# Optimization experiments

Measured on AMD Instinct MI355X. Metric: run time of the kernel, lower is better.

Reference implementation:

```python
import jax, jax.numpy as jnp
import numpy as np

D_MODEL = 2048
NUM_HEADS = 32
D_HEAD = D_MODEL // NUM_HEADS
L = 2048


def setup_inputs() -> dict:
    key = jax.random.key(0)
    ks = jax.random.split(key, 9)
    s = 0.02  # init scale
    return {
        "X": jax.random.normal(ks[0], (L, D_MODEL), dtype=jnp.float32),
        "Wq_w": jax.random.normal(ks[1], (D_MODEL, D_MODEL), jnp.float32) * s,
        "Wq_b": jax.random.normal(ks[2], (D_MODEL,), jnp.float32) * s,
        "Wk_w": jax.random.normal(ks[3], (D_MODEL, D_MODEL), jnp.float32) * s,
        "Wk_b": jax.random.normal(ks[4], (D_MODEL,), jnp.float32) * s,
        "Wv_w": jax.random.normal(ks[5], (D_MODEL, D_MODEL), jnp.float32) * s,
        "Wv_b": jax.random.normal(ks[6], (D_MODEL,), jnp.float32) * s,
        "Wo_w": jax.random.normal(ks[7], (D_MODEL, D_MODEL), jnp.float32) * s,
        "Wo_b": jax.random.normal(ks[8], (D_MODEL,), jnp.float32) * s,
    }


def reference(X, Wq_w, Wq_b, Wk_w, Wk_b, Wv_w, Wv_b, Wo_w, Wo_b):
    # torch.nn.Linear: y = x @ W.T + b
    seq = X.shape[0]
    Q = (X @ Wq_w.T + Wq_b).reshape(seq, D_HEAD, NUM_HEADS)  # (L, d, h)
    K = (X @ Wk_w.T + Wk_b).reshape(seq, D_HEAD, NUM_HEADS)
    V = (X @ Wv_w.T + Wv_b).reshape(seq, D_HEAD, NUM_HEADS)
    # scores[l, m, h] = sum_d Q[l,d,h] * K[m,d,h]; note scale is sqrt(d_model),
    # faithful to the source (not sqrt(d_head)).
    scores = jnp.einsum('ldh,mdh->lmh', Q, K) / jnp.sqrt(jnp.float32(D_MODEL))
    attn = jax.nn.softmax(scores, axis=1)  # softmax over key axis m
    out = jnp.einsum('lmh,mdh->ldh', attn, V).reshape(seq, D_MODEL)
    return out @ Wo_w.T + Wo_b
```

## Files before the change

### kernel.cpp

```cpp
#include <hip/hip_runtime.h>
#include <hip/hip_bf16.h>
#include <stdint.h>
#include <stddef.h>

#define L_SEQ   2048
#define DM      2048
#define NH      32
#define DH      64
#define QSCALE  0.02209708691207961f
#define QS2     0.0318793579f
#define MAT_N   (L_SEQ * DM)

typedef __bf16  bf16x8 __attribute__((ext_vector_type(8)));
typedef float   f32x4  __attribute__((ext_vector_type(4)));
typedef __hip_bfloat16 bf16;

#if __has_builtin(__builtin_amdgcn_exp2f)
#define EXP2F(x) __builtin_amdgcn_exp2f(x)
#else
#define EXP2F(x) __expf((x) * 0.6931471805599453f)
#endif

__device__ __forceinline__ void gl_lds16(const bf16* g, bf16* l) {
    __builtin_amdgcn_global_load_lds(
        (const __attribute__((address_space(1))) unsigned int*)g,
        (__attribute__((address_space(3))) unsigned int*)l,
        16, 0, 0);
}

__device__ __forceinline__ void conv8s(const float* src, bf16* dst, int i, float sc) {
    float4 a = *(const float4*)(src + i);
    float4 b = *(const float4*)(src + i + 4);
    union { bf16 h[8]; uint4 u; } pk;
    pk.h[0] = __float2bfloat16(a.x * sc); pk.h[1] = __float2bfloat16(a.y * sc);
    pk.h[2] = __float2bfloat16(a.z * sc); pk.h[3] = __float2bfloat16(a.w * sc);
    pk.h[4] = __float2bfloat16(b.x * sc); pk.h[5] = __float2bfloat16(b.y * sc);
    pk.h[6] = __float2bfloat16(b.z * sc); pk.h[7] = __float2bfloat16(b.w * sc);
    *(uint4*)(dst + i) = pk.u;
}

__global__ __launch_bounds__(256)
void convert4_kernel(const float* __restrict__ s0, const float* __restrict__ s1,
                     const float* __restrict__ s2, const float* __restrict__ s3,
                     bf16* __restrict__ d0, bf16* __restrict__ d1,
                     bf16* __restrict__ d2, bf16* __restrict__ d3)
{
    const float* s; bf16* d; float sc = 1.0f;
    switch (blockIdx.y) {
        case 0:  s = s0; d = d0; break;
        case 1:  s = s1; d = d1; sc = QS2; break;
        case 2:  s = s2; d = d2; break;
        default: s = s3; d = d3; break;
    }
    const int i = (blockIdx.x * 256 + threadIdx.x) * 8;
    conv8s(s, d, i, sc);
}

__global__ __launch_bounds__(256)
void convert_wo_perm_kernel(const float* __restrict__ s, bf16* __restrict__ d)
{
    const int t   = blockIdx.x * 256 + threadIdx.x;
    const int row = t >> 8;
    const int k0  = (t & 255) * 8;
    const float* sr = s + (size_t)row * DM;
    union { bf16 h[8]; uint4 u; } pk;
#pragma unroll
    for (int j = 0; j < 8; ++j) {
        const int kp = k0 + j;
        const int k  = ((kp & 63) << 5) | (kp >> 6);
        pk.h[j] = __float2bfloat16(sr[k]);
    }
    *(uint4*)(d + (size_t)row * DM + k0) = pk.u;
}

__global__ __launch_bounds__(512)
void qkv8_gemm_kernel(const bf16* __restrict__ Xb,
                      const bf16* __restrict__ Wq, const float* __restrict__ bq,
                      const bf16* __restrict__ Wk, const float* __restrict__ bk,
                      const bf16* __restrict__ Wv, const float* __restrict__ bv,
                      bf16* __restrict__ Qws, bf16* __restrict__ Kws, bf16* __restrict__ Vws,
                      const float* __restrict__ WoSrc, bf16* __restrict__ WobDst)
{
    __shared__ bf16 lds[2 * 32768];

    const int bid = blockIdx.x;
    const int tid  = threadIdx.x;

    if (bid >= 192) {
        const int t = (bid - 192) * 512 + tid;
        const int row = t >> 4;
        const int k0base = (t & 15) * 128;
        const float* sr = WoSrc + (size_t)row * DM;
        bf16* dr = WobDst + (size_t)row * DM;
        for (int i = 0; i < 16; ++i) {
            const int k0 = k0base + i * 8;
            union { bf16 h[8]; uint4 u; } pk;
#pragma unroll
            for (int j = 0; j < 8; ++j) {
                const int kp = k0 + j;
                const int k  = ((kp & 63) << 5) | (kp >> 6);
                pk.h[j] = __float2bfloat16(sr[k]);
            }
            *(uint4*)(dr + k0) = pk.u;
        }
        return;
    }

    const int mt  = bid & 7;
    const int nt  = bid >> 3;
    const int m0  = mt << 8;
    const int ng0 = nt << 8;
    const int z   = ng0 >> 11;
    const int n0  = ng0 & 2047;
    const bf16*  W    = (z == 0) ? Wq : (z == 1) ? Wk : Wv;
    const float* bias = (z == 0) ? bq : (z == 1) ? bk : bv;

    const int lane = tid & 63;
    const int wave = tid >> 6;
    const int wm   = wave >> 2;
    const int wn   = wave & 3;
    const int grp8 = (lane >> 4) * 8;
    const int grp4 = (lane >> 4) * 4;
    const int l15  = lane & 15;
    const int axor = (l15 & 7) << 3;

    const int scol = ((tid & 7) * 8) ^ (((tid >> 3) & 7) << 3);
    const bf16* gb[8];
    int loff[8];
#pragma unroll
    for (int e = 0; e < 8; ++e) {
        const int hh  = e >> 1;
        const int row = (e & 1) * 64 + (tid >> 3);
        loff[e] = hh * 8192 + (e & 1) * 4096 + tid * 8;
        if (hh < 2) {
            gb[e] = Xb + (size_t)(m0 + hh * 128 + row) * DM + scol;
        } else {
            const int nn   = n0 + (hh - 2) * 128 + row;
            const int brow = ((nn & 63) << 5) | (nn >> 6);
            gb[e] = W + (size_t)brow * DM + scol;
        }
    }

    const bool swap  = (z == 2);
    const int  aside = swap ? 16384 : 0;
    const int  bside = swap ? 0 : 16384;
    const bf16* fa0 = lds + aside + wm * 8192 + l15 * 64;
    const bf16* fb0 = lds + bside + (wn >> 1) * 8192 + ((wn & 1) * 64 + l15) * 64;

    f32x4 acc[8][4];
    const f32x4 zero = {0.f, 0.f, 0.f, 0.f};
#pragma unroll
    for (int i = 0; i < 8; ++i)
#pragma unroll
        for (int j = 0; j < 4; ++j) acc[i][j] = zero;

#pragma unroll
    for (int e = 0; e < 8; ++e) gl_lds16(gb[e],      lds + loff[e]);
#pragma unroll
    for (int e = 0; e < 8; ++e) gl_lds16(gb[e] + 64, lds + 32768 + loff[e]);
    asm volatile("s_waitcnt vmcnt(8)" ::: "memory");
    asm volatile("s_barrier" ::: "memory");

    for (int t = 0; t < 32; ++t) {
        const int cb = (t & 1) << 15;
        const bf16* fa = fa0 + cb;
        const bf16* fb = fb0 + cb;
        const int c0 = grp8 ^ axor;
        const int c1 = (32 + grp8) ^ axor;

        bf16x8 af[8], bfr[4];
#pragma unroll
        for (int i = 0; i < 8; ++i) af[i] = *(const bf16x8*)(fa + i * 1024 + c0);
#pragma unroll
        for (int j = 0; j < 4; ++j) bfr[j] = *(const bf16x8*)(fb + j * 1024 + c0);
        asm volatile("s_barrier" ::: "memory");
        __builtin_amdgcn_s_setprio(1);
#pragma unroll
        for (int i = 0; i < 8; ++i)
#pragma unroll
            for (int j = 0; j < 4; ++j)
                acc[i][j] = __builtin_amdgcn_mfma_f32_16x16x32_bf16(af[i], bfr[j], acc[i][j], 0, 0, 0);
        __builtin_amdgcn_s_setprio(0);

#pragma unroll
        for (int i = 0; i < 8; ++i) af[i] = *(const bf16x8*)(fa + i * 1024 + c1);
#pragma unroll
        for (int j = 0; j < 4; ++j) bfr[j] = *(const bf16x8*)(fb + j * 1024 + c1);
        asm volatile("s_waitcnt lgkmcnt(0)" ::: "memory");
        asm volatile("s_barrier" ::: "memory");
        if (t + 2 < 32) {
            const int kb2 = (t + 2) << 6;
#pragma unroll
            for (int e = 0; e < 8; ++e)
                gl_lds16(gb[e] + kb2, lds + cb + loff[e]);
            asm volatile("s_waitcnt vmcnt(8)" ::: "memory");
        } else if (t == 30) {
            asm volatile("s_waitcnt vmcnt(0)" ::: "memory");
        }
        __builtin_amdgcn_s_setprio(1);
#pragma unroll
        for (int i = 0; i < 8; ++i)
#pragma unroll
            for (int j = 0; j < 4; ++j)
                acc[i][j] = __builtin_amdgcn_mfma_f32_16x16x32_bf16(af[i], bfr[j], acc[i][j], 0, 0, 0);
        __builtin_amdgcn_s_setprio(0);
        asm volatile("s_barrier" ::: "memory");
    }

    if (z == 0) {
#pragma unroll
        for (int j = 0; j < 4; ++j) {
            const int np = n0 + wn * 64 + j * 16 + l15;
            const float bb = bias[((np & 63) << 5) | (np >> 6)] * QS2;
            const size_t base = ((size_t)(np >> 6) * L_SEQ) * DH + (np & 63);
#pragma unroll
            for (int i = 0; i < 8; ++i)
#pragma unroll
                for (int r = 0; r < 4; ++r) {
                    const int m = m0 + wm * 128 + i * 16 + grp4 + r;
                    Qws[base + (size_t)m * DH] = __float2bfloat16(acc[i][j][r] + bb);
                }
        }
    } else if (z == 1) {
#pragma unroll
        for (int j = 0; j < 4; ++j) {
            const int np = n0 + wn * 64 + j * 16 + l15;
            const float bb = bias[((np & 63) << 5) | (np >> 6)];
            const size_t base = ((size_t)(np >> 6) * L_SEQ) * DH + (np & 63);
#pragma unroll
            for (int i = 0; i < 8; ++i)
#pragma unroll
                for (int r = 0; r < 4; ++r) {
                    const int m = m0 + wm * 128 + i * 16 + grp4 + r;
                    Kws[base + (size_t)m * DH] = __float2bfloat16(acc[i][j][r] + bb);
                }
        }
    } else {
#pragma unroll
        for (int i = 0; i < 8; ++i)
#pragma unroll
            for (int r = 0; r < 4; ++r) {
                const int np = n0 + wm * 128 + i * 16 + grp4 + r;
                const float bb = bias[((np & 63) << 5) | (np >> 6)];
#pragma unroll
                for (int j = 0; j < 4; ++j) {
                    const int mcol = m0 + wn * 64 + j * 16 + l15;
                    Vws[(size_t)np * L_SEQ + mcol] = __float2bfloat16(acc[i][j][r] + bb);
                }
            }
    }
}

__global__ __launch_bounds__(256)
void out_fused_kernel(const bf16* __restrict__ A,
                      const bf16* __restrict__ Wo,
                      const float* __restrict__ bo,
                      float* __restrict__ out)
{
    __shared__ bf16 lds[2 * 16384];

    const int m0 = blockIdx.y * 128, n0 = blockIdx.x * 128;
    const int tid  = threadIdx.x;
    const int lane = tid & 63;
    const int wave = tid >> 6;
    const int wr   = (wave >> 1) * 64;
    const int wc   = (wave & 1) * 64;
    const int grp8 = (lane >> 4) * 8;
    const int grp4 = (lane >> 4) * 4;
    const int l15  = lane & 15;
    const int axor = (l15 & 7) << 3;

    const bf16* gb[8]; int loff[8];
#pragma unroll
    for (int e = 0; e < 8; ++e) {
        const int idx = (e & 3) * 256 + tid;
        const int row = idx >> 3;
        const int sc  = ((idx & 7) * 8) ^ ((row & 7) << 3);
        if (e < 4) { gb[e] = A  + (size_t)(m0 + row) * DM + sc; loff[e] = idx * 8; }
        else       { gb[e] = Wo + (size_t)(n0 + row) * DM + sc; loff[e] = 8192 + idx * 8; }
    }

    f32x4 acc[4][4];
    const f32x4 zero = {0.f, 0.f, 0.f, 0.f};
#pragma unroll
    for (int i = 0; i < 4; ++i)
#pragma unroll
        for (int j = 0; j < 4; ++j) acc[i][j] = zero;

#pragma unroll
    for (int e = 0; e < 8; ++e) gl_lds16(gb[e],      lds + loff[e]);
#pragma unroll
    for (int e = 0; e < 8; ++e) gl_lds16(gb[e] + 64, lds + 16384 + loff[e]);
    asm volatile("s_waitcnt vmcnt(8)" ::: "memory");
    asm volatile("s_barrier" ::: "memory");

    for (int t = 0; t < 32; ++t) {
        const int cb = (t & 1) << 14;
        const bf16* fa = lds + cb;
        const bf16* fb = lds + cb + 8192;
        const int c0 = grp8 ^ axor;
        const int c1 = (32 + grp8) ^ axor;

        bf16x8 af[4], bfr[4];
#pragma unroll
        for (int i = 0; i < 4; ++i) af[i]  = *(const bf16x8*)(fa + (wr + i * 16 + l15) * 64 + c0);
#pragma unroll
        for (int j = 0; j < 4; ++j) bfr[j] = *(const bf16x8*)(fb + (wc + j * 16 + l15) * 64 + c0);
        asm volatile("s_barrier" ::: "memory");
        __builtin_amdgcn_s_setprio(1);
#pragma unroll
        for (int i = 0; i < 4; ++i)
#pragma unroll
            for (int j = 0; j < 4; ++j)
                acc[i][j] = __builtin_amdgcn_mfma_f32_16x16x32_bf16(af[i], bfr[j], acc[i][j], 0, 0, 0);
        __builtin_amdgcn_s_setprio(0);

#pragma unroll
        for (int i = 0; i < 4; ++i) af[i]  = *(const bf16x8*)(fa + (wr + i * 16 + l15) * 64 + c1);
#pragma unroll
        for (int j = 0; j < 4; ++j) bfr[j] = *(const bf16x8*)(fb + (wc + j * 16 + l15) * 64 + c1);
        asm volatile("s_waitcnt lgkmcnt(0)" ::: "memory");
        asm volatile("s_barrier" ::: "memory");
        if (t + 2 < 32) {
            const int kadv = (t + 2) * 64;
#pragma unroll
            for (int e = 0; e < 8; ++e) gl_lds16(gb[e] + kadv, lds + cb + loff[e]);
            asm volatile("s_waitcnt vmcnt(8)" ::: "memory");
        } else if (t == 30) {
            asm volatile("s_waitcnt vmcnt(0)" ::: "memory");
        }
        __builtin_amdgcn_s_setprio(1);
#pragma unroll
        for (int i = 0; i < 4; ++i)
#pragma unroll
            for (int j = 0; j < 4; ++j)
                acc[i][j] = __builtin_amdgcn_mfma_f32_16x16x32_bf16(af[i], bfr[j], acc[i][j], 0, 0, 0);
        __builtin_amdgcn_s_setprio(0);
        asm volatile("s_barrier" ::: "memory");
    }

#pragma unroll
    for (int j = 0; j < 4; ++j) {
        const int n = n0 + wc + j * 16 + l15;
        const float bb = bo[n];
#pragma unroll
        for (int i = 0; i < 4; ++i) {
#pragma unroll
            for (int r = 0; r < 4; ++r) {
                const int m = m0 + wr + i * 16 + grp4 + r;
                out[(size_t)m * DM + n] = acc[i][j][r] + bb;
            }
        }
    }
}

__global__ __launch_bounds__(512)
void attention_kernel(const bf16* __restrict__ Qws,
                      const bf16* __restrict__ Kws,
                      const bf16* __restrict__ Vws,
                      bf16* __restrict__ Attn)
{
    __shared__ bf16 lds[24576];

    const int h = blockIdx.x, qb = blockIdx.y;
    const int tid  = threadIdx.x;
    const int wave = tid >> 6;
    const int lane = tid & 63;
    const int grp  = lane >> 4;
    const int l15  = lane & 15;
    const int grp8 = grp * 8;
    const int axor = (l15 & 7) << 3;

    const bf16* Qh = Qws + (size_t)h * L_SEQ * DH;
    const bf16* Kh = Kws + (size_t)h * L_SEQ * DH;
    const bf16* Vh = Vws + (size_t)h * DH * L_SEQ;

    const int q0 = qb * 128 + wave * 16;

    bf16x8 qf0 = *(const bf16x8*)(Qh + (size_t)(q0 + l15) * DH + grp8);
    bf16x8 qf1 = *(const bf16x8*)(Qh + (size_t)(q0 + l15) * DH + 32 + grp8);

    const int srow = tid >> 3;
    const int scol = ((tid & 7) * 8) ^ ((srow & 7) << 3);
    const bf16* gK = Kh + (size_t)srow * DH + scol;
    const bf16* gV = Vh + (size_t)srow * L_SEQ + scol;
    bf16* ldsK = lds + tid * 8;
    bf16* ldsV = lds + 8192 + tid * 8;
    bf16* Plds = lds + 16384;
    const int prow = (wave * 16 + l15) * 64;

    const f32x4 zero = {0.f, 0.f, 0.f, 0.f};
    f32x4 Oacc[4];
#pragma unroll
    for (int t = 0; t < 4; ++t) Oacc[t] = zero;
    float lsum = 0.f;

    gl_lds16(gK,        ldsK);
    gl_lds16(gV,        ldsV);
    gl_lds16(gK + 4096, ldsK + 4096);
    gl_lds16(gV + 64,   ldsV + 4096);
    asm volatile("s_waitcnt vmcnt(2)" ::: "memory");
    asm volatile("s_barrier" ::: "memory");

    for (int kb = 0; kb < 32; ++kb) {
        const int cb = (kb & 1) << 12;
        const bf16* Kc = lds + cb;
        const bf16* Vc = lds + 8192 + cb;

#pragma unroll
        for (int t = 0; t < 4; ++t) {
            const int rr = (t * 16 + l15) * 64;
            bf16x8 k0 = *(const bf16x8*)(Kc + rr + (grp8 ^ axor));
            bf16x8 k1 = *(const bf16x8*)(Kc + rr + ((32 + grp8) ^ axor));
            f32x4 s = zero;
            __builtin_amdgcn_s_setprio(1);
            s = __builtin_amdgcn_mfma_f32_16x16x32_bf16(k0, qf0, s, 0, 0, 0);
            s = __builtin_amdgcn_mfma_f32_16x16x32_bf16(k1, qf1, s, 0, 0, 0);
            __builtin_amdgcn_s_setprio(0);
            float p0 = EXP2F(s[0]), p1 = EXP2F(s[1]),
                  p2 = EXP2F(s[2]), p3 = EXP2F(s[3]);
            lsum += (p0 + p1) + (p2 + p3);
            union { bf16 hh[4]; uint2 u; } pk;
            pk.hh[0] = __float2bfloat16(p0); pk.hh[1] = __float2bfloat16(p1);
            pk.hh[2] = __float2bfloat16(p2); pk.hh[3] = __float2bfloat16(p3);
            *(uint2*)(&Plds[prow + ((t * 16 + grp * 4) ^ axor)]) = pk.u;
        }
        asm volatile("s_waitcnt lgkmcnt(0)" ::: "memory");

        __builtin_amdgcn_s_setprio(1);
#pragma unroll
        for (int ks = 0; ks < 2; ++ks) {
            bf16x8 pa = *(const bf16x8*)(&Plds[prow + ((ks * 32 + grp8) ^ axor)]);
#pragma unroll
            for (int t = 0; t < 4; ++t) {
                bf16x8 vb = *(const bf16x8*)(Vc + (t * 16 + l15) * 64 + ((ks * 32 + grp8) ^ axor));
                Oacc[t] = __builtin_amdgcn_mfma_f32_16x16x32_bf16(pa, vb, Oacc[t], 0, 0, 0);
            }
        }
        __builtin_amdgcn_s_setprio(0);

        asm volatile("s_waitcnt lgkmcnt(0)" ::: "memory");
        asm volatile("s_barrier" ::: "memory");
        if (kb + 2 < 32) {
            gl_lds16(gK + (kb + 2) * 4096, ldsK + cb);
            gl_lds16(gV + (kb + 2) * 64,   ldsV + cb);
            asm volatile("s_waitcnt vmcnt(2)" ::: "memory");
        } else if (kb == 30) {
            asm volatile("s_waitcnt vmcnt(0)" ::: "memory");
        }
        asm volatile("s_barrier" ::: "memory");
    }

    float sden = lsum;
    sden += __shfl_xor(sden, 16, 64);
    sden += __shfl_xor(sden, 32, 64);
    const float inv = 1.f / sden;
    float invs[4];
#pragma unroll
    for (int r = 0; r < 4; ++r)
        invs[r] = __shfl(inv, grp * 4 + r, 64);

#pragma unroll
    for (int t = 0; t < 4; ++t) {
#pragma unroll
        for (int r = 0; r < 4; ++r) {
            const int m = q0 + grp * 4 + r;
            const int d = t * 16 + l15;
            Attn[(size_t)m * DM + h * 64 + d] = __float2bfloat16(Oacc[t][r] * invs[r]);
        }
    }
}

extern "C" void kernel_launch(void* const* d_in, const int* in_sizes, int n_in,
                              void* d_out, int out_size, void* d_ws, size_t ws_size,
                              hipStream_t stream)
{
    const float* X  = (const float*)d_in[0];
    const float* Wq = (const float*)d_in[1];
    const float* bq = (const float*)d_in[2];
    const float* Wk = (const float*)d_in[3];
    const float* bk = (const float*)d_in[4];
    const float* Wv = (const float*)d_in[5];
    const float* bv = (const float*)d_in[6];
    const float* Wo = (const float*)d_in[7];
    const float* bo = (const float*)d_in[8];
    float* out = (float*)d_out;

    bf16* Xb   = (bf16*)d_ws;
    bf16* Wqb  = Xb  + (size_t)MAT_N;
    bf16* Wkb  = Wqb + (size_t)MAT_N;
    bf16* Wvb  = Wkb + (size_t)MAT_N;
    bf16* Qws  = Wvb + (size_t)MAT_N;
    bf16* Kws  = Qws + (size_t)MAT_N;
    bf16* Vws  = Kws + (size_t)MAT_N;
    bf16* Wob7 = Vws + (size_t)MAT_N;
    bf16* Attn = Wqb;

    const bool big = ws_size >= (size_t)8 * MAT_N * sizeof(bf16);
    bf16* Wob = big ? Wob7 : Xb;

    convert4_kernel<<<dim3(2048, 4), 256, 0, stream>>>(X, Wq, Wk, Wv, Xb, Wqb, Wkb, Wvb);
    if (big) {
        qkv8_gemm_kernel<<<dim3(256), 512, 0, stream>>>(Xb, Wqb, bq, Wkb, bk, Wvb, bv,
                                                        Qws, Kws, Vws, Wo, Wob7);
    } else {
        qkv8_gemm_kernel<<<dim3(192), 512, 0, stream>>>(Xb, Wqb, bq, Wkb, bk, Wvb, bv,
                                                        Qws, Kws, Vws, Wo, Wob);
        convert_wo_perm_kernel<<<dim3(2048), 256, 0, stream>>>(Wo, Wob);
    }
    attention_kernel<<<dim3(32, 16), 512, 0, stream>>>(Qws, Kws, Vws, Attn);
    out_fused_kernel<<<dim3(16, 16), 256, 0, stream>>>(Attn, Wob, bo, out);
}
```

Measured before the change: 249.9 us.

## Use a four-slot K/V LDS ring and process two key tiles per barrier

The attention kernel's K/V staging grows from a double buffer to a four-slot ring in LDS. Each loop iteration now consumes two 64-key tiles between barriers and then prefetches the next two tiles. This is meant to halve the barrier and wait count and to keep more global-to-LDS loads in flight. In exchange, LDS per block rises from 48 KB to 80 KB, which may lower the number of resident blocks per CU.

Result: no change. 249.7 us (median of 2 runs) (-0.1%).

```diff
diff --git a/kernel.cpp b/kernel.cpp
--- a/kernel.cpp
+++ b/kernel.cpp
@@ -360,7 +360,7 @@
                       const bf16* __restrict__ Vws,
                       bf16* __restrict__ Attn)
 {
-    __shared__ bf16 lds[24576];
+    __shared__ bf16 lds[40960];
 
     const int h = blockIdx.x, qb = blockIdx.y;
     const int tid  = threadIdx.x;
@@ -384,9 +384,7 @@
     const int scol = ((tid & 7) * 8) ^ ((srow & 7) << 3);
     const bf16* gK = Kh + (size_t)srow * DH + scol;
     const bf16* gV = Vh + (size_t)srow * L_SEQ + scol;
-    bf16* ldsK = lds + tid * 8;
-    bf16* ldsV = lds + 8192 + tid * 8;
-    bf16* Plds = lds + 16384;
+    bf16* Plds = lds + 32768;
     const int prow = (wave * 16 + l15) * 64;
 
     const f32x4 zero = {0.f, 0.f, 0.f, 0.f};
@@ -395,57 +393,65 @@
     for (int t = 0; t < 4; ++t) Oacc[t] = zero;
     float lsum = 0.f;
 
-    gl_lds16(gK,        ldsK);
-    gl_lds16(gV,        ldsV);
-    gl_lds16(gK + 4096, ldsK + 4096);
-    gl_lds16(gV + 64,   ldsV + 4096);
-    asm volatile("s_waitcnt vmcnt(2)" ::: "memory");
+#pragma unroll
+    for (int s = 0; s < 4; ++s) {
+        gl_lds16(gK + s * 4096, lds + s * 4096 + tid * 8);
+        gl_lds16(gV + s * 64,   lds + 16384 + s * 4096 + tid * 8);
+    }
+    asm volatile("s_waitcnt vmcnt(4)" ::: "memory");
     asm volatile("s_barrier" ::: "memory");
 
-    for (int kb = 0; kb < 32; ++kb) {
-        const int cb = (kb & 1) << 12;
-        const bf16* Kc = lds + cb;
-        const bf16* Vc = lds + 8192 + cb;
-
-#pragma unroll
-        for (int t = 0; t < 4; ++t) {
-            const int rr = (t * 16 + l15) * 64;
-            bf16x8 k0 = *(const bf16x8*)(Kc + rr + (grp8 ^ axor));
-            bf16x8 k1 = *(const bf16x8*)(Kc + rr + ((32 + grp8) ^ axor));
-            f32x4 s = zero;
+    for (int i = 0; i < 16; ++i) {
+#pragma unroll
+        for (int half = 0; half < 2; ++half) {
+            const int u  = 2 * i + half;
+            const bf16* Kc = lds + (u & 3) * 4096;
+            const bf16* Vc = lds + 16384 + (u & 3) * 4096;
+
+#pragma unroll
+            for (int t = 0; t < 4; ++t) {
+                const int rr = (t * 16 + l15) * 64;
+                bf16x8 k0 = *(const bf16x8*)(Kc + rr + (grp8 ^ axor));
+                bf16x8 k1 = *(const bf16x8*)(Kc + rr + ((32 + grp8) ^ axor));
+                f32x4 s = zero;
+                __builtin_amdgcn_s_setprio(1);
+                s = __builtin_amdgcn_mfma_f32_16x16x32_bf16(k0, qf0, s, 0, 0, 0);
+                s = __builtin_amdgcn_mfma_f32_16x16x32_bf16(k1, qf1, s, 0, 0, 0);
+                __builtin_amdgcn_s_setprio(0);
+                float p0 = EXP2F(s[0]), p1 = EXP2F(s[1]),
+                      p2 = EXP2F(s[2]), p3 = EXP2F(s[3]);
+                lsum += (p0 + p1) + (p2 + p3);
+                union { bf16 hh[4]; uint2 u2; } pk;
+                pk.hh[0] = __float2bfloat16(p0); pk.hh[1] = __float2bfloat16(p1);
+                pk.hh[2] = __float2bfloat16(p2); pk.hh[3] = __float2bfloat16(p3);
+                *(uint2*)(&Plds[prow + ((t * 16 + grp * 4) ^ axor)]) = pk.u2;
+            }
+            asm volatile("s_waitcnt lgkmcnt(0)" ::: "memory");
+
             __builtin_amdgcn_s_setprio(1);
-            s = __builtin_amdgcn_mfma_f32_16x16x32_bf16(k0, qf0, s, 0, 0, 0);
-            s = __builtin_amdgcn_mfma_f32_16x16x32_bf16(k1, qf1, s, 0, 0, 0);
+#pragma unroll
+            for (int ks = 0; ks < 2; ++ks) {
+                bf16x8 pa = *(const bf16x8*)(&Plds[prow + ((ks * 32 + grp8) ^ axor)]);
+#pragma unroll
+                for (int t = 0; t < 4; ++t) {
+                    bf16x8 vb = *(const bf16x8*)(Vc + (t * 16 + l15) * 64 + ((ks * 32 + grp8) ^ axor));
+                    Oacc[t] = __builtin_amdgcn_mfma_f32_16x16x32_bf16(pa, vb, Oacc[t], 0, 0, 0);
+                }
+            }
             __builtin_amdgcn_s_setprio(0);
-            float p0 = EXP2F(s[0]), p1 = EXP2F(s[1]),
-                  p2 = EXP2F(s[2]), p3 = EXP2F(s[3]);
-            lsum += (p0 + p1) + (p2 + p3);
-            union { bf16 hh[4]; uint2 u; } pk;
-            pk.hh[0] = __float2bfloat16(p0); pk.hh[1] = __float2bfloat16(p1);
-            pk.hh[2] = __float2bfloat16(p2); pk.hh[3] = __float2bfloat16(p3);
-            *(uint2*)(&Plds[prow + ((t * 16 + grp * 4) ^ axor)]) = pk.u;
-        }
-        asm volatile("s_waitcnt lgkmcnt(0)" ::: "memory");
-
-        __builtin_amdgcn_s_setprio(1);
-#pragma unroll
-        for (int ks = 0; ks < 2; ++ks) {
-            bf16x8 pa = *(const bf16x8*)(&Plds[prow + ((ks * 32 + grp8) ^ axor)]);
-#pragma unroll
-            for (int t = 0; t < 4; ++t) {
-                bf16x8 vb = *(const bf16x8*)(Vc + (t * 16 + l15) * 64 + ((ks * 32 + grp8) ^ axor));
-                Oacc[t] = __builtin_amdgcn_mfma_f32_16x16x32_bf16(pa, vb, Oacc[t], 0, 0, 0);
+            asm volatile("s_waitcnt lgkmcnt(0)" ::: "memory");
+        }
+
+        asm volatile("s_barrier" ::: "memory");
+        if (i + 2 < 16) {
+            const int u2 = 2 * i + 4;
+#pragma unroll
+            for (int s = 0; s < 2; ++s) {
+                gl_lds16(gK + (size_t)(u2 + s) * 4096, lds + ((u2 + s) & 3) * 4096 + tid * 8);
+                gl_lds16(gV + (u2 + s) * 64,           lds + 16384 + ((u2 + s) & 3) * 4096 + tid * 8);
             }
-        }
-        __builtin_amdgcn_s_setprio(0);
-
-        asm volatile("s_waitcnt lgkmcnt(0)" ::: "memory");
-        asm volatile("s_barrier" ::: "memory");
-        if (kb + 2 < 32) {
-            gl_lds16(gK + (kb + 2) * 4096, ldsK + cb);
-            gl_lds16(gV + (kb + 2) * 64,   ldsV + cb);
-            asm volatile("s_waitcnt vmcnt(2)" ::: "memory");
-        } else if (kb == 30) {
+            asm volatile("s_waitcnt vmcnt(4)" ::: "memory");
+        } else if (i == 14) {
             asm volatile("s_waitcnt vmcnt(0)" ::: "memory");
         }
         asm volatile("s_barrier" ::: "memory");
```
